# Optimization experiments

Measured on AMD Instinct MI355X. Metric: run time of the kernel, lower is better.

Reference implementation:

```python
import jax, jax.numpy as jnp
import numpy as np

E, T, D, H = 32, 65536, 512, 1024


def setup_inputs() -> dict:
    key = jax.random.key(0)
    k = jax.random.split(key, 7)
    norm = lambda kk, shp, sc: (jax.random.normal(kk, shp, jnp.float32) * sc)
    x = norm(k[0], (T, D), 1.0)
    w1 = norm(k[1], (E, D, H), D ** -0.5)   # per-expert up-proj (gate branch)
    b1 = norm(k[2], (E, H), 0.02)
    w3 = norm(k[3], (E, D, H), D ** -0.5)   # per-expert up-proj (linear branch)
    b3 = norm(k[4], (E, H), 0.02)
    w2 = norm(k[5], (E, H, D), H ** -0.5)   # per-expert down-proj
    b2 = norm(k[6], (E, D), 0.02)
    # tokens are pre-sorted by expert; uniform dispatch of T//E tokens per expert
    group_sizes = jnp.full((E,), T // E, jnp.int32)
    return dict(x=x, w1=w1, b1=b1, w3=w3, b3=b3, w2=w2, b2=b2,
                group_sizes=group_sizes)


def reference(x, w1, b1, w3, b3, w2, b2, group_sizes):
    # expert id per token, derived from contiguous group sizes
    bounds = jnp.cumsum(group_sizes)                       # [E]
    seg = jnp.searchsorted(bounds, jnp.arange(x.shape[0]), side='right')  # [T]
    # grouped GEMMs: per-expert weight bank applied to its contiguous token slab
    h1 = jax.lax.ragged_dot(x, w1, group_sizes) + b1[seg]  # [T,H]
    h3 = jax.lax.ragged_dot(x, w3, group_sizes) + b3[seg]  # [T,H]
    h = jax.nn.silu(h1) * h3                               # SwiGLU gate
    out = jax.lax.ragged_dot(h, w2, group_sizes) + b2[seg] # [T,D]
    return out
```

## Files before the change

kernel.cpp:

```cpp
#include <hip/hip_runtime.h>
#include <hip/hip_bf16.h>

#define TOK 65536
#define NE  32
#define DD  512
#define HH  1024
#define TPE 2048

typedef short s16x8  __attribute__((ext_vector_type(8)));
typedef float f32x16 __attribute__((ext_vector_type(16)));
using u16 = unsigned short;
using u32 = unsigned int;

__device__ __forceinline__ u16 f2bf(float f) {
  __bf16 h = (__bf16)f;
  return __builtin_bit_cast(u16, h);
}
__device__ __forceinline__ u32 pk2(float lo, float hi) {
  return (u32)f2bf(lo) | ((u32)f2bf(hi) << 16);
}
__device__ __forceinline__ int swz(int row, int colb) {
  return (row << 7) + (colb ^ ((row & 7) << 4));
}

#define MFMA(a, b, c) __builtin_amdgcn_mfma_f32_32x32x16_bf16(a, b, c, 0, 0, 0)
#define GLD(src, dst) __builtin_amdgcn_global_load_lds( \
    (const __attribute__((address_space(1))) void*)(src), \
    (__attribute__((address_space(3))) void*)(dst), 16, 0, 0)
#define SETP(n) __builtin_amdgcn_s_setprio(n)
#define SCHEDB() __builtin_amdgcn_sched_barrier(0)
#define SBAR()  __builtin_amdgcn_s_barrier()

__global__ __launch_bounds__(256) void p1_cvt_x(
    const float* __restrict__ x, u16* __restrict__ xb) {
  const size_t i = ((size_t)blockIdx.x * 256 + threadIdx.x) * 8;
  const float4 a = *(const float4*)(x + i);
  const float4 b = *(const float4*)(x + i + 4);
  uint4 v;
  v.x = pk2(a.x, a.y); v.y = pk2(a.z, a.w);
  v.z = pk2(b.x, b.y); v.w = pk2(b.z, b.w);
  *(uint4*)(xb + i) = v;
}

__global__ __launch_bounds__(256) void p2_w13t(
    const float* __restrict__ w1, const float* __restrict__ w3,
    u16* __restrict__ w13t) {
  __shared__ __align__(16) u16 L1[64 * 72], L3[64 * 72];
  const int bid = blockIdx.x;
  const int e = bid >> 7, rr = bid & 127;
  const int d0 = (rr & 7) << 6, h0 = (rr >> 3) << 6;
  const int t = threadIdx.x;
  const float* const s1 = w1 + (size_t)e * DD * HH + (size_t)d0 * HH + h0;
  const float* const s3 = w3 + (size_t)e * DD * HH + (size_t)d0 * HH + h0;
  const int cg = (t & 15) << 2, rbase = t >> 4;
#pragma unroll
  for (int j = 0; j < 4; ++j) {
    const int dr = rbase + (j << 4);
    const float4 a = *(const float4*)(s1 + (size_t)dr * HH + cg);
    const float4 b = *(const float4*)(s3 + (size_t)dr * HH + cg);
    L1[(cg + 0) * 72 + dr] = f2bf(a.x); L1[(cg + 1) * 72 + dr] = f2bf(a.y);
    L1[(cg + 2) * 72 + dr] = f2bf(a.z); L1[(cg + 3) * 72 + dr] = f2bf(a.w);
    L3[(cg + 0) * 72 + dr] = f2bf(b.x); L3[(cg + 1) * 72 + dr] = f2bf(b.y);
    L3[(cg + 2) * 72 + dr] = f2bf(b.z); L3[(cg + 3) * 72 + dr] = f2bf(b.w);
  }
  __syncthreads();
  u16* const dst = w13t + (size_t)e * (2 * HH) * DD;
  const int cb8 = (t & 7) << 3;
#pragma unroll
  for (int j = 0; j < 2; ++j) {
    const int nloc = (t >> 3) + (j << 5);
    const int n = h0 + nloc;
    const int R1 = ((n >> 5) << 6) + (n & 31);
    const uint4 v1 = *(const uint4*)(L1 + nloc * 72 + cb8);
    const uint4 v3 = *(const uint4*)(L3 + nloc * 72 + cb8);
    *(uint4*)(dst + (size_t)R1 * DD + d0 + cb8) = v1;
    *(uint4*)(dst + (size_t)(R1 + 32) * DD + d0 + cb8) = v3;
  }
}

__global__ __launch_bounds__(256) void p3_w2t(
    const float* __restrict__ w2, u16* __restrict__ w2t) {
  __shared__ __align__(16) u16 L[64 * 72];
  const int bid = blockIdx.x;
  const int e = bid >> 7, rr = bid & 127;
  const int d0 = (rr & 7) << 6, h0 = (rr >> 3) << 6;
  const int t = threadIdx.x;
  const float* const s = w2 + (size_t)e * HH * DD + (size_t)h0 * DD + d0;
  const int cg = (t & 15) << 2, rbase = t >> 4;
#pragma unroll
  for (int j = 0; j < 4; ++j) {
    const int hr = rbase + (j << 4);
    const float4 a = *(const float4*)(s + (size_t)hr * DD + cg);
    L[(cg + 0) * 72 + hr] = f2bf(a.x); L[(cg + 1) * 72 + hr] = f2bf(a.y);
    L[(cg + 2) * 72 + hr] = f2bf(a.z); L[(cg + 3) * 72 + hr] = f2bf(a.w);
  }
  __syncthreads();
  u16* const dst = w2t + (size_t)e * DD * HH;
  const int cb8 = (t & 7) << 3;
#pragma unroll
  for (int j = 0; j < 2; ++j) {
    const int dloc = (t >> 3) + (j << 5);
    const uint4 v = *(const uint4*)(L + dloc * 72 + cb8);
    *(uint4*)(dst + (size_t)(d0 + dloc) * HH + h0 + cb8) = v;
  }
}

__global__ __launch_bounds__(256, 3) void g0_up(
    const u16* __restrict__ A, const u16* __restrict__ Bm,
    const float* __restrict__ bx, const float* __restrict__ by,
    u16* __restrict__ hp) {
  constexpr int K = DD;
  __shared__ __align__(16) char lds[32768];
  char* const As = lds;
  char* const Bs = lds + 16384;

  int bid = blockIdx.x;
  bid = (bid & 7) * (NE * 256 / 8) + (bid >> 3);
  const int e   = bid >> 8;
  const int rr  = bid & 255;
  const int m_t = rr & 15;
  const int n_t = rr >> 4;
  const int rowbase = e * TPE + (m_t << 7);

  const int t = threadIdx.x, wv = t >> 6, lane = t & 63;
  const int l31 = lane & 31, half = lane >> 5;
  const int wm = wv >> 1, wn = wv & 1;

  const u16* const Abase = A + (size_t)rowbase * K;
  const u16* const Bbase = Bm + ((size_t)e * 2048 + (size_t)n_t * 128) * K;

  int soff[4], lb[4];
#pragma unroll
  for (int j = 0; j < 4; ++j) {
    const int idx = (j << 8) + t;
    const int r = idx >> 3;
    const int cb = ((idx & 7) << 4) ^ ((r & 7) << 4);
    soff[j] = r * K + (cb >> 1);
    lb[j] = ((j << 8) + (wv << 6)) << 4;
  }

  f32x16 c00 = {}, c01 = {}, c10 = {}, c11 = {};
  const int sw  = (l31 & 7) << 4;
  const int ra0 = ((wm << 6) + l31) << 7, ra1 = ra0 + (32 << 7);
  const int rb0 = ((wn << 6) + l31) << 7, rb1 = rb0 + (32 << 7);

  for (int kt = 0; kt < 8; ++kt) {
    const u16* const Ak = Abase + (kt << 6);
    const u16* const Bk = Bbase + (kt << 6);
#pragma unroll
    for (int j = 0; j < 4; ++j) {
      GLD(Ak + soff[j], As + lb[j]);
      GLD(Bk + soff[j], Bs + lb[j]);
    }
    __syncthreads();
#pragma unroll
    for (int ks = 0; ks < 4; ++ks) {
      const int ko = ((ks << 5) + (half << 4)) ^ sw;
      const s16x8 a0 = *(const s16x8*)(As + ra0 + ko);
      const s16x8 a1 = *(const s16x8*)(As + ra1 + ko);
      const s16x8 b0 = *(const s16x8*)(Bs + rb0 + ko);
      const s16x8 b1 = *(const s16x8*)(Bs + rb1 + ko);
      c00 = MFMA(a0, b0, c00); c01 = MFMA(a0, b1, c01);
      c10 = MFMA(a1, b0, c10); c11 = MFMA(a1, b1, c11);
    }
    __syncthreads();
  }

  const int hcol = (n_t << 6) + (wn << 5) + l31;
  const float bv1 = bx[e * HH + hcol];
  const float bv3 = by[e * HH + hcol];
#pragma unroll
  for (int mf = 0; mf < 2; ++mf) {
    const f32x16 A1 = mf ? c10 : c00;
    const f32x16 A3 = mf ? c11 : c01;
#pragma unroll
    for (int rg = 0; rg < 16; ++rg) {
      const int grow = rowbase + (wm << 6) + (mf << 5) +
                       (rg & 3) + ((rg >> 2) << 3) + (half << 2);
      const float s1 = A1[rg] + bv1;
      const float s3 = A3[rg] + bv3;
      hp[(size_t)grow * HH + hcol] = f2bf(s1 * s3 / (1.0f + __expf(-s1)));
    }
  }
}

__global__ __launch_bounds__(512, 2) void g1_down(
    const u16* __restrict__ A, const u16* __restrict__ Bm,
    const float* __restrict__ bx, float* __restrict__ op) {
  constexpr int K  = HH;
  constexpr int NT = K >> 6;
  constexpr int NB = 2;
  constexpr int NWG = NE * 8 * NB;
  __shared__ __align__(16) char lds[131072];

  int bid = blockIdx.x;
  bid = (bid & 7) * (NWG / 8) + (bid >> 3);
  const int e   = bid / (8 * NB);
  const int rr  = bid % (8 * NB);
  const int m_t = rr & 7;
  const int n_t = rr >> 3;
  const int rowbase = e * TPE + (m_t << 8);

  const int t = threadIdx.x;
  const int wv = t >> 6, lane = t & 63;
  const int l31 = lane & 31, half = lane >> 5;
  const int wm = wv >> 2, wn = wv & 3;

  const u16* const Abase = A + (size_t)rowbase * K;
  const u16* const Bbase = Bm + ((size_t)e * NB + n_t) * 256 * K;

  int srcoff0, srcoff1;
  {
    const int c0 = t,       lr0 = c0 >> 3, s0 = (c0 & 7) ^ (lr0 & 7);
    const int c1 = 512 + t, lr1 = c1 >> 3, s1 = (c1 & 7) ^ (lr1 & 7);
    srcoff0 = ((lr0 << 1) | (s0 >> 2)) * K + ((s0 & 3) << 3);
    srcoff1 = ((lr1 << 1) | (s1 >> 2)) * K + ((s1 & 3) << 3);
  }
  const int t16 = t << 4;

  auto stageQ = [&](int tau, int q) {
    const u16* const src = ((q & 1) ? Bbase : Abase) + tau * 64 + (q >> 1) * 32;
    char* const dst = lds + ((tau & 1) << 16) + (q << 14);
    GLD(src + srcoff0, dst + t16);
    GLD(src + srcoff1, dst + 8192 + t16);
  };

  const int lrow_off = l31 >> 1;
  const int pbit = l31 & 1;
  const int sw7 = lrow_off & 7;
  const int sA0 = (((pbit << 2) | 0 | half) ^ sw7) << 4;
  const int sA1 = (((pbit << 2) | 2 | half) ^ sw7) << 4;
  const int aoff = ((wm << 6) + lrow_off) << 7;
  const int boff = ((wn << 5) + lrow_off) << 7;

  f32x16 acc[4][2] = {};
  s16x8 b00{}, b01{}, b10{}, b11{};

#define VM4 asm volatile("s_waitcnt vmcnt(4)" ::: "memory")
#define VM0 asm volatile("s_waitcnt vmcnt(0)" ::: "memory")
#define LGKM0 asm volatile("s_waitcnt lgkmcnt(0)" ::: "memory")
#define NOPV ((void)0)

#define PHASE(CB, KH, MH, DOB, STG, VM) do { \
  const char* const Aq = (CB) + ((KH) << 15); \
  const char* const Bq = Aq + 16384; \
  if (DOB) { \
    b00 = *(const s16x8*)(Bq + boff + 0 * 2048 + sA0); \
    b01 = *(const s16x8*)(Bq + boff + 1 * 2048 + sA0); \
    b10 = *(const s16x8*)(Bq + boff + 0 * 2048 + sA1); \
    b11 = *(const s16x8*)(Bq + boff + 1 * 2048 + sA1); \
  } \
  const s16x8 a0 = *(const s16x8*)(Aq + aoff + (2 * (MH)) * 2048 + sA0); \
  const s16x8 a1 = *(const s16x8*)(Aq + aoff + (2 * (MH)) * 2048 + sA1); \
  const s16x8 a2 = *(const s16x8*)(Aq + aoff + (2 * (MH) + 1) * 2048 + sA0); \
  const s16x8 a3 = *(const s16x8*)(Aq + aoff + (2 * (MH) + 1) * 2048 + sA1); \
  STG; VM; \
  SCHEDB(); SBAR(); LGKM0; SCHEDB(); \
  SETP(1); \
  acc[2 * (MH)][0]     = MFMA(a0, b00, acc[2 * (MH)][0]); \
  acc[2 * (MH)][1]     = MFMA(a0, b01, acc[2 * (MH)][1]); \
  acc[2 * (MH)][0]     = MFMA(a1, b10, acc[2 * (MH)][0]); \
  acc[2 * (MH)][1]     = MFMA(a1, b11, acc[2 * (MH)][1]); \
  acc[2 * (MH) + 1][0] = MFMA(a2, b00, acc[2 * (MH) + 1][0]); \
  acc[2 * (MH) + 1][1] = MFMA(a2, b01, acc[2 * (MH) + 1][1]); \
  acc[2 * (MH) + 1][0] = MFMA(a3, b10, acc[2 * (MH) + 1][0]); \
  acc[2 * (MH) + 1][1] = MFMA(a3, b11, acc[2 * (MH) + 1][1]); \
  SETP(0); \
} while (0)

  stageQ(0, 0); stageQ(0, 1); stageQ(0, 2); stageQ(0, 3);
  VM4; SCHEDB(); SBAR();

  for (int kt = 0; kt < NT - 1; ++kt) {
    const char* const cb = lds + ((kt & 1) << 16);
    PHASE(cb, 0, 0, true,  (stageQ(kt + 1, 0), stageQ(kt + 1, 1)), NOPV);
    PHASE(cb, 0, 1, false, NOPV, VM4);
    PHASE(cb, 1, 0, true,  (stageQ(kt + 1, 2), stageQ(kt + 1, 3)), NOPV);
    PHASE(cb, 1, 1, false, NOPV, VM4);
  }
  {
    const char* const cb = lds + (((NT - 1) & 1) << 16);
    PHASE(cb, 0, 0, true,  NOPV, NOPV);
    PHASE(cb, 0, 1, false, NOPV, VM0);
    PHASE(cb, 1, 0, true,  NOPV, NOPV);
    PHASE(cb, 1, 1, false, NOPV, NOPV);
  }

#undef PHASE
#undef VM4
#undef VM0
#undef LGKM0
#undef NOPV

#pragma unroll
  for (int mf = 0; mf < 4; ++mf) {
#pragma unroll
    for (int nf = 0; nf < 2; ++nf) {
      const int col = (n_t << 8) + (wn << 6) + (nf << 5) + l31;
      const float bv = bx[e * DD + col];
#pragma unroll
      for (int rg = 0; rg < 16; ++rg) {
        const int grow = rowbase + (wm << 7) + (mf << 5) +
                         (rg & 3) + ((rg >> 2) << 3) + (half << 2);
        op[(size_t)grow * DD + col] = acc[mf][nf][rg] + bv;
      }
    }
  }
}

__global__ __launch_bounds__(256, 2) void k1_up_swiglu(
    const float* __restrict__ x,  const float* __restrict__ w1,
    const float* __restrict__ b1, const float* __restrict__ w3,
    const float* __restrict__ b3, u16* __restrict__ hbuf) {
  __shared__ __align__(16) char lds[32768];
  char* const As  = lds;
  char* const B1s = lds + 16384;
  char* const B3s = lds + 24576;
  const int bid = blockIdx.x;
  const int e = bid >> 8, rr = bid & 255;
  const int m_t = rr & 15, n_t = rr >> 4;
  const int rowbase = e * TPE + (m_t << 7), colbase = n_t << 6;
  const int t = threadIdx.x, wv = t >> 6, lane = t & 63;
  const int l31 = lane & 31, half = lane >> 5;
  const int wm = wv >> 1, wn = wv & 1;
  const int ag = t & 15, am0 = t >> 4, bn = t & 63, bk0 = t >> 6;
  const float* const xb = x + (size_t)rowbase * DD + (ag << 2);
  const size_t woff = (size_t)e * (DD * HH) + colbase + bn;
  const float* const w1b = w1 + woff;
  const float* const w3b = w3 + woff;
  float4 ra[8]; float rb1[16], rb3[16];
  auto gload = [&](int kt) {
    const float* xp = xb + (kt << 6);
#pragma unroll
    for (int j = 0; j < 8; ++j)
      ra[j] = *(const float4*)(xp + (size_t)(am0 + (j << 4)) * DD);
#pragma unroll
    for (int j = 0; j < 2; ++j) {
      const int k0 = (kt << 6) + ((bk0 + (j << 2)) << 3);
#pragma unroll
      for (int i = 0; i < 8; ++i) {
        rb1[(j << 3) + i] = w1b[(size_t)(k0 + i) * HH];
        rb3[(j << 3) + i] = w3b[(size_t)(k0 + i) * HH];
      }
    }
  };
  f32x16 acc10 = {}, acc11 = {}, acc30 = {}, acc31 = {};
  gload(0);
  for (int kt = 0; kt < 8; ++kt) {
    if (kt) __syncthreads();
#pragma unroll
    for (int j = 0; j < 8; ++j) {
      const int m = am0 + (j << 4);
      uint2 v; v.x = pk2(ra[j].x, ra[j].y); v.y = pk2(ra[j].z, ra[j].w);
      *(uint2*)(As + swz(m, ag << 3)) = v;
    }
#pragma unroll
    for (int j = 0; j < 2; ++j) {
      const int kg = bk0 + (j << 2);
      uint4 v;
      v.x = pk2(rb1[(j << 3) + 0], rb1[(j << 3) + 1]);
      v.y = pk2(rb1[(j << 3) + 2], rb1[(j << 3) + 3]);
      v.z = pk2(rb1[(j << 3) + 4], rb1[(j << 3) + 5]);
      v.w = pk2(rb1[(j << 3) + 6], rb1[(j << 3) + 7]);
      *(uint4*)(B1s + swz(bn, kg << 4)) = v;
      v.x = pk2(rb3[(j << 3) + 0], rb3[(j << 3) + 1]);
      v.y = pk2(rb3[(j << 3) + 2], rb3[(j << 3) + 3]);
      v.z = pk2(rb3[(j << 3) + 4], rb3[(j << 3) + 5]);
      v.w = pk2(rb3[(j << 3) + 6], rb3[(j << 3) + 7]);
      *(uint4*)(B3s + swz(bn, kg << 4)) = v;
    }
    __syncthreads();
    if (kt < 7) gload(kt + 1);
#pragma unroll
    for (int kk = 0; kk < 4; ++kk) {
      const int colb = (kk << 5) + (half << 4);
      const s16x8 a0 = *(const s16x8*)(As  + swz((wm << 6) + l31,      colb));
      const s16x8 a1 = *(const s16x8*)(As  + swz((wm << 6) + 32 + l31, colb));
      const s16x8 f1 = *(const s16x8*)(B1s + swz((wn << 5) + l31,      colb));
      const s16x8 f3 = *(const s16x8*)(B3s + swz((wn << 5) + l31,      colb));
      acc10 = MFMA(a0, f1, acc10); acc30 = MFMA(a0, f3, acc30);
      acc11 = MFMA(a1, f1, acc11); acc31 = MFMA(a1, f3, acc31);
    }
  }
  const int gcol = colbase + (wn << 5) + l31;
  const float bv1 = b1[e * HH + gcol], bv3 = b3[e * HH + gcol];
  u16* const hp = hbuf + gcol;
#pragma unroll
  for (int mb = 0; mb < 2; ++mb) {
    const f32x16 A1 = mb ? acc11 : acc10;
    const f32x16 A3 = mb ? acc31 : acc30;
#pragma unroll
    for (int rg = 0; rg < 16; ++rg) {
      const int grow = rowbase + (wm << 6) + (mb << 5) +
                       (rg & 3) + ((rg >> 2) << 3) + (half << 2);
      const float s1 = A1[rg] + bv1, s3 = A3[rg] + bv3;
      hp[(size_t)grow * HH] = f2bf(s1 * s3 / (1.0f + __expf(-s1)));
    }
  }
}

__global__ __launch_bounds__(256, 2) void k2_down(
    const u16* __restrict__ hbuf, const float* __restrict__ w2,
    const float* __restrict__ b2, float* __restrict__ out) {
  __shared__ __align__(16) char lds[32768];
  char* const As = lds;
  char* const Bs = lds + 16384;
  const int bid = blockIdx.x;
  const int e = bid >> 6, rr = bid & 63;
  const int m_t = rr & 15, n_t = rr >> 4;
  const int rowbase = e * TPE + (m_t << 7), colbase = n_t << 7;
  const int t = threadIdx.x, wv = t >> 6, lane = t & 63;
  const int l31 = lane & 31, half = lane >> 5;
  const int wm = wv >> 1, wn = wv & 1;
  const int ag = t & 7, am0 = t >> 3, bnn = t & 127, bk0 = t >> 7;
  const u16* const hb = hbuf + (size_t)rowbase * HH + (ag << 3);
  const float* const w2b = w2 + (size_t)e * (HH * DD) + colbase + bnn;
  uint4 ra[4]; float rb[32];
  auto gload = [&](int kt) {
#pragma unroll
    for (int j = 0; j < 4; ++j)
      ra[j] = *(const uint4*)(hb + (size_t)(am0 + (j << 5)) * HH + (kt << 6));
#pragma unroll
    for (int j = 0; j < 4; ++j) {
      const int k0 = (kt << 6) + ((bk0 + (j << 1)) << 3);
#pragma unroll
      for (int i = 0; i < 8; ++i)
        rb[(j << 3) + i] = w2b[(size_t)(k0 + i) * DD];
    }
  };
  f32x16 c00 = {}, c01 = {}, c10 = {}, c11 = {};
  gload(0);
  for (int kt = 0; kt < 16; ++kt) {
    if (kt) __syncthreads();
#pragma unroll
    for (int j = 0; j < 4; ++j)
      *(uint4*)(As + swz(am0 + (j << 5), ag << 4)) = ra[j];
#pragma unroll
    for (int j = 0; j < 4; ++j) {
      const int kg = bk0 + (j << 1);
      uint4 v;
      v.x = pk2(rb[(j << 3) + 0], rb[(j << 3) + 1]);
      v.y = pk2(rb[(j << 3) + 2], rb[(j << 3) + 3]);
      v.z = pk2(rb[(j << 3) + 4], rb[(j << 3) + 5]);
      v.w = pk2(rb[(j << 3) + 6], rb[(j << 3) + 7]);
      *(uint4*)(Bs + swz(bnn, kg << 4)) = v;
    }
    __syncthreads();
    if (kt < 15) gload(kt + 1);
#pragma unroll
    for (int kk = 0; kk < 4; ++kk) {
      const int colb = (kk << 5) + (half << 4);
      const s16x8 af0 = *(const s16x8*)(As + swz((wm << 6) + l31,      colb));
      const s16x8 af1 = *(const s16x8*)(As + swz((wm << 6) + 32 + l31, colb));
      const s16x8 bf0 = *(const s16x8*)(Bs + swz((wn << 6) + l31,      colb));
      const s16x8 bf1 = *(const s16x8*)(Bs + swz((wn << 6) + 32 + l31, colb));
      c00 = MFMA(af0, bf0, c00); c01 = MFMA(af0, bf1, c01);
      c10 = MFMA(af1, bf0, c10); c11 = MFMA(af1, bf1, c11);
    }
  }
#pragma unroll
  for (int mb = 0; mb < 2; ++mb) {
#pragma unroll
    for (int nb = 0; nb < 2; ++nb) {
      const f32x16 c = mb ? (nb ? c11 : c10) : (nb ? c01 : c00);
      const int gcol = colbase + (wn << 6) + (nb << 5) + l31;
      const float bv = b2[e * DD + gcol];
#pragma unroll
      for (int rg = 0; rg < 16; ++rg) {
        const int grow = rowbase + (wm << 6) + (mb << 5) +
                         (rg & 3) + ((rg >> 2) << 3) + (half << 2);
        out[(size_t)grow * DD + gcol] = c[rg] + bv;
      }
    }
  }
}

extern "C" void kernel_launch(void* const* d_in, const int* in_sizes, int n_in,
                              void* d_out, int out_size, void* d_ws, size_t ws_size,
                              hipStream_t stream) {
  const float* x  = (const float*)d_in[0];
  const float* w1 = (const float*)d_in[1];
  const float* b1 = (const float*)d_in[2];
  const float* w3 = (const float*)d_in[3];
  const float* b3 = (const float*)d_in[4];
  const float* w2 = (const float*)d_in[5];
  const float* b2 = (const float*)d_in[6];

  const size_t W13T_B = (size_t)NE * 2 * HH * DD * 2;
  const size_t W2T_B  = (size_t)NE * DD * HH * 2;
  const size_t H_B    = (size_t)TOK * HH * 2;

  if (ws_size >= W13T_B + W2T_B + H_B) {
    u16* const xb   = (u16*)d_out;
    u16* const w13t = (u16*)d_ws;
    u16* const w2t  = (u16*)((char*)d_ws + W13T_B);
    u16* const hbuf = (u16*)((char*)d_ws + W13T_B + W2T_B);

    p1_cvt_x<<<dim3(TOK * DD / 2048), dim3(256), 0, stream>>>(x, xb);
    p2_w13t <<<dim3(NE * 128),        dim3(256), 0, stream>>>(w1, w3, w13t);
    p3_w2t  <<<dim3(NE * 128),        dim3(256), 0, stream>>>(w2, w2t);
    g0_up  <<<dim3(NE * 256), dim3(256), 0, stream>>>(xb, w13t, b1, b3, hbuf);
    g1_down<<<dim3(NE * 16),  dim3(512), 0, stream>>>(hbuf, w2t, b2, (float*)d_out);
  } else {
    u16* hbuf = (ws_size >= H_B) ? (u16*)d_ws : (u16*)d_out;
    k1_up_swiglu<<<dim3(NE * 256), dim3(256), 0, stream>>>(x, w1, b1, w3, b3, hbuf);
    k2_down<<<dim3(NE * 64), dim3(256), 0, stream>>>(hbuf, w2, b2, (float*)d_out);
  }
}
```

Before: 354.8 us.

## Fuse x bf16 conversion into up-proj GEMM and merge weight transpose kernels

Removes the separate x fp32->bf16 conversion kernel: g0_up now loads fp32 x into registers, converts it, and writes swizzled bf16 into LDS. The next A tile is prefetched during the MFMA loop, and the trailing barrier is replaced by one at the top of the next iteration. The two weight transpose kernels are merged into a single launch. This drops a launch and the write/read of the bf16 x copy, but each up-proj block now rereads x as fp32, doubling A traffic across the 8 N-tiles, and the registers held for the prefetch may limit occupancy.

```diff
diff --git a/kernel.cpp b/kernel.cpp
--- a/kernel.cpp
+++ b/kernel.cpp
@@ -31,82 +31,68 @@
 #define SCHEDB() __builtin_amdgcn_sched_barrier(0)
 #define SBAR()  __builtin_amdgcn_s_barrier()
 
-__global__ __launch_bounds__(256) void p1_cvt_x(
-    const float* __restrict__ x, u16* __restrict__ xb) {
-  const size_t i = ((size_t)blockIdx.x * 256 + threadIdx.x) * 8;
-  const float4 a = *(const float4*)(x + i);
-  const float4 b = *(const float4*)(x + i + 4);
-  uint4 v;
-  v.x = pk2(a.x, a.y); v.y = pk2(a.z, a.w);
-  v.z = pk2(b.x, b.y); v.w = pk2(b.z, b.w);
-  *(uint4*)(xb + i) = v;
-}
-
-__global__ __launch_bounds__(256) void p2_w13t(
+__global__ __launch_bounds__(256) void p23_wt(
     const float* __restrict__ w1, const float* __restrict__ w3,
-    u16* __restrict__ w13t) {
+    const float* __restrict__ w2,
+    u16* __restrict__ w13t, u16* __restrict__ w2t) {
   __shared__ __align__(16) u16 L1[64 * 72], L3[64 * 72];
-  const int bid = blockIdx.x;
-  const int e = bid >> 7, rr = bid & 127;
-  const int d0 = (rr & 7) << 6, h0 = (rr >> 3) << 6;
+  const int bid0 = blockIdx.x;
   const int t = threadIdx.x;
-  const float* const s1 = w1 + (size_t)e * DD * HH + (size_t)d0 * HH + h0;
-  const float* const s3 = w3 + (size_t)e * DD * HH + (size_t)d0 * HH + h0;
   const int cg = (t & 15) << 2, rbase = t >> 4;
-#pragma unroll
-  for (int j = 0; j < 4; ++j) {
-    const int dr = rbase + (j << 4);
-    const float4 a = *(const float4*)(s1 + (size_t)dr * HH + cg);
-    const float4 b = *(const float4*)(s3 + (size_t)dr * HH + cg);
-    L1[(cg + 0) * 72 + dr] = f2bf(a.x); L1[(cg + 1) * 72 + dr] = f2bf(a.y);
-    L1[(cg + 2) * 72 + dr] = f2bf(a.z); L1[(cg + 3) * 72 + dr] = f2bf(a.w);
-    L3[(cg + 0) * 72 + dr] = f2bf(b.x); L3[(cg + 1) * 72 + dr] = f2bf(b.y);
-    L3[(cg + 2) * 72 + dr] = f2bf(b.z); L3[(cg + 3) * 72 + dr] = f2bf(b.w);
-  }
-  __syncthreads();
-  u16* const dst = w13t + (size_t)e * (2 * HH) * DD;
   const int cb8 = (t & 7) << 3;
-#pragma unroll
-  for (int j = 0; j < 2; ++j) {
-    const int nloc = (t >> 3) + (j << 5);
-    const int n = h0 + nloc;
-    const int R1 = ((n >> 5) << 6) + (n & 31);
-    const uint4 v1 = *(const uint4*)(L1 + nloc * 72 + cb8);
-    const uint4 v3 = *(const uint4*)(L3 + nloc * 72 + cb8);
-    *(uint4*)(dst + (size_t)R1 * DD + d0 + cb8) = v1;
-    *(uint4*)(dst + (size_t)(R1 + 32) * DD + d0 + cb8) = v3;
-  }
-}
-
-__global__ __launch_bounds__(256) void p3_w2t(
-    const float* __restrict__ w2, u16* __restrict__ w2t) {
-  __shared__ __align__(16) u16 L[64 * 72];
-  const int bid = blockIdx.x;
-  const int e = bid >> 7, rr = bid & 127;
-  const int d0 = (rr & 7) << 6, h0 = (rr >> 3) << 6;
-  const int t = threadIdx.x;
-  const float* const s = w2 + (size_t)e * HH * DD + (size_t)h0 * DD + d0;
-  const int cg = (t & 15) << 2, rbase = t >> 4;
-#pragma unroll
-  for (int j = 0; j < 4; ++j) {
-    const int hr = rbase + (j << 4);
-    const float4 a = *(const float4*)(s + (size_t)hr * DD + cg);
-    L[(cg + 0) * 72 + hr] = f2bf(a.x); L[(cg + 1) * 72 + hr] = f2bf(a.y);
-    L[(cg + 2) * 72 + hr] = f2bf(a.z); L[(cg + 3) * 72 + hr] = f2bf(a.w);
-  }
-  __syncthreads();
-  u16* const dst = w2t + (size_t)e * DD * HH;
-  const int cb8 = (t & 7) << 3;
-#pragma unroll
-  for (int j = 0; j < 2; ++j) {
-    const int dloc = (t >> 3) + (j << 5);
-    const uint4 v = *(const uint4*)(L + dloc * 72 + cb8);
-    *(uint4*)(dst + (size_t)(d0 + dloc) * HH + h0 + cb8) = v;
+
+  if (bid0 < NE * 128) {
+    const int e = bid0 >> 7, rr = bid0 & 127;
+    const int d0 = (rr & 7) << 6, h0 = (rr >> 3) << 6;
+    const float* const s1 = w1 + (size_t)e * DD * HH + (size_t)d0 * HH + h0;
+    const float* const s3 = w3 + (size_t)e * DD * HH + (size_t)d0 * HH + h0;
+#pragma unroll
+    for (int j = 0; j < 4; ++j) {
+      const int dr = rbase + (j << 4);
+      const float4 a = *(const float4*)(s1 + (size_t)dr * HH + cg);
+      const float4 b = *(const float4*)(s3 + (size_t)dr * HH + cg);
+      L1[(cg + 0) * 72 + dr] = f2bf(a.x); L1[(cg + 1) * 72 + dr] = f2bf(a.y);
+      L1[(cg + 2) * 72 + dr] = f2bf(a.z); L1[(cg + 3) * 72 + dr] = f2bf(a.w);
+      L3[(cg + 0) * 72 + dr] = f2bf(b.x); L3[(cg + 1) * 72 + dr] = f2bf(b.y);
+      L3[(cg + 2) * 72 + dr] = f2bf(b.z); L3[(cg + 3) * 72 + dr] = f2bf(b.w);
+    }
+    __syncthreads();
+    u16* const dst = w13t + (size_t)e * (2 * HH) * DD;
+#pragma unroll
+    for (int j = 0; j < 2; ++j) {
+      const int nloc = (t >> 3) + (j << 5);
+      const int n = h0 + nloc;
+      const int R1 = ((n >> 5) << 6) + (n & 31);
+      const uint4 v1 = *(const uint4*)(L1 + nloc * 72 + cb8);
+      const uint4 v3 = *(const uint4*)(L3 + nloc * 72 + cb8);
+      *(uint4*)(dst + (size_t)R1 * DD + d0 + cb8) = v1;
+      *(uint4*)(dst + (size_t)(R1 + 32) * DD + d0 + cb8) = v3;
+    }
+  } else {
+    const int bid = bid0 - NE * 128;
+    const int e = bid >> 7, rr = bid & 127;
+    const int d0 = (rr & 7) << 6, h0 = (rr >> 3) << 6;
+    const float* const s = w2 + (size_t)e * HH * DD + (size_t)h0 * DD + d0;
+#pragma unroll
+    for (int j = 0; j < 4; ++j) {
+      const int hr = rbase + (j << 4);
+      const float4 a = *(const float4*)(s + (size_t)hr * DD + cg);
+      L1[(cg + 0) * 72 + hr] = f2bf(a.x); L1[(cg + 1) * 72 + hr] = f2bf(a.y);
+      L1[(cg + 2) * 72 + hr] = f2bf(a.z); L1[(cg + 3) * 72 + hr] = f2bf(a.w);
+    }
+    __syncthreads();
+    u16* const dst = w2t + (size_t)e * DD * HH;
+#pragma unroll
+    for (int j = 0; j < 2; ++j) {
+      const int dloc = (t >> 3) + (j << 5);
+      const uint4 v = *(const uint4*)(L1 + dloc * 72 + cb8);
+      *(uint4*)(dst + (size_t)(d0 + dloc) * HH + h0 + cb8) = v;
+    }
   }
 }
 
 __global__ __launch_bounds__(256, 3) void g0_up(
-    const u16* __restrict__ A, const u16* __restrict__ Bm,
+    const float* __restrict__ x, const u16* __restrict__ Bm,
     const float* __restrict__ bx, const float* __restrict__ by,
     u16* __restrict__ hp) {
   constexpr int K = DD;
@@ -126,9 +112,18 @@
   const int l31 = lane & 31, half = lane >> 5;
   const int wm = wv >> 1, wn = wv & 1;
 
-  const u16* const Abase = A + (size_t)rowbase * K;
+  const int ag  = t & 15;
+  const int am0 = t >> 4;
+  const float* const xb = x + (size_t)rowbase * K + (ag << 2);
+  float4 ra[8];
+  auto loadA = [&](int kt) {
+    const float* xp = xb + (kt << 6);
+#pragma unroll
+    for (int j = 0; j < 8; ++j)
+      ra[j] = *(const float4*)(xp + (size_t)(am0 + (j << 4)) * K);
+  };
+
   const u16* const Bbase = Bm + ((size_t)e * 2048 + (size_t)n_t * 128) * K;
-
   int soff[4], lb[4];
 #pragma unroll
   for (int j = 0; j < 4; ++j) {
@@ -144,15 +139,20 @@
   const int ra0 = ((wm << 6) + l31) << 7, ra1 = ra0 + (32 << 7);
   const int rb0 = ((wn << 6) + l31) << 7, rb1 = rb0 + (32 << 7);
 
+  loadA(0);
   for (int kt = 0; kt < 8; ++kt) {
-    const u16* const Ak = Abase + (kt << 6);
+    if (kt) __syncthreads();
+#pragma unroll
+    for (int j = 0; j < 8; ++j) {
+      const int m = am0 + (j << 4);
+      uint2 v; v.x = pk2(ra[j].x, ra[j].y); v.y = pk2(ra[j].z, ra[j].w);
+      *(uint2*)(As + swz(m, ag << 3)) = v;
+    }
     const u16* const Bk = Bbase + (kt << 6);
 #pragma unroll
-    for (int j = 0; j < 4; ++j) {
-      GLD(Ak + soff[j], As + lb[j]);
-      GLD(Bk + soff[j], Bs + lb[j]);
-    }
+    for (int j = 0; j < 4; ++j) GLD(Bk + soff[j], Bs + lb[j]);
     __syncthreads();
+    if (kt < 7) loadA(kt + 1);
 #pragma unroll
     for (int ks = 0; ks < 4; ++ks) {
       const int ko = ((ks << 5) + (half << 4)) ^ sw;
@@ -163,7 +163,6 @@
       c00 = MFMA(a0, b0, c00); c01 = MFMA(a0, b1, c01);
       c10 = MFMA(a1, b0, c10); c11 = MFMA(a1, b1, c11);
     }
-    __syncthreads();
   }
 
   const int hcol = (n_t << 6) + (wn << 5) + l31;
@@ -491,15 +490,12 @@
   const size_t H_B    = (size_t)TOK * HH * 2;
 
   if (ws_size >= W13T_B + W2T_B + H_B) {
-    u16* const xb   = (u16*)d_out;
     u16* const w13t = (u16*)d_ws;
     u16* const w2t  = (u16*)((char*)d_ws + W13T_B);
     u16* const hbuf = (u16*)((char*)d_ws + W13T_B + W2T_B);
 
-    p1_cvt_x<<<dim3(TOK * DD / 2048), dim3(256), 0, stream>>>(x, xb);
-    p2_w13t <<<dim3(NE * 128),        dim3(256), 0, stream>>>(w1, w3, w13t);
-    p3_w2t  <<<dim3(NE * 128),        dim3(256), 0, stream>>>(w2, w2t);
-    g0_up  <<<dim3(NE * 256), dim3(256), 0, stream>>>(xb, w13t, b1, b3, hbuf);
+    p23_wt <<<dim3(NE * 256), dim3(256), 0, stream>>>(w1, w3, w2, w13t, w2t);
+    g0_up  <<<dim3(NE * 256), dim3(256), 0, stream>>>(x, w13t, b1, b3, hbuf);
     g1_down<<<dim3(NE * 16),  dim3(512), 0, stream>>>(hbuf, w2t, b2, (float*)d_out);
   } else {
     u16* hbuf = (ws_size >= H_B) ? (u16*)d_ws : (u16*)d_out;
```

Result: slower. 387.5 us (+9.2%).
